# Optimization experiments

Measured on AMD Instinct MI355X. Metric: run time of the kernel, lower is better.

Reference implementation:

```python
import jax, jax.numpy as jnp
import numpy as np

D_MODEL = 1024
N_HEADS = 16
D_K = D_MODEL // N_HEADS
SCALE = float(np.sqrt(D_K))


def depthwise3(x, w, b):
    # x: [B, S, D]; w: [D, 3] (PyTorch Conv1d weight [D,1,3] squeezed); b: [D]
    # cross-correlation with kernel_size=3, padding=1, groups=D
    xp = jnp.pad(x, ((0, 0), (1, 1), (0, 0)))
    return xp[:, :-2] * w[:, 0] + xp[:, 1:-1] * w[:, 1] + xp[:, 2:] * w[:, 2] + b


def setup_inputs() -> dict:
    key = jax.random.key(0)
    ks = jax.random.split(key, 16)
    B, S, D = 2, 2048, D_MODEL
    s_lin = 1.0 / np.sqrt(D)
    s_dw = 1.0 / np.sqrt(3)
    inp = {
        "x": jax.random.normal(ks[0], (B, S, D), dtype=jnp.float32),
        "dwq_w": jax.random.uniform(ks[1], (D, 3), jnp.float32, -s_dw, s_dw),
        "dwq_b": jax.random.uniform(ks[2], (D,), jnp.float32, -s_dw, s_dw),
        "dwk_w": jax.random.uniform(ks[3], (D, 3), jnp.float32, -s_dw, s_dw),
        "dwk_b": jax.random.uniform(ks[4], (D,), jnp.float32, -s_dw, s_dw),
        "dwv_w": jax.random.uniform(ks[5], (D, 3), jnp.float32, -s_dw, s_dw),
        "dwv_b": jax.random.uniform(ks[6], (D,), jnp.float32, -s_dw, s_dw),
        "wq": jax.random.uniform(ks[7], (D, D), jnp.float32, -s_lin, s_lin),
        "bq": jax.random.uniform(ks[8], (D,), jnp.float32, -s_lin, s_lin),
        "wk": jax.random.uniform(ks[9], (D, D), jnp.float32, -s_lin, s_lin),
        "bk": jax.random.uniform(ks[10], (D,), jnp.float32, -s_lin, s_lin),
        "wv": jax.random.uniform(ks[11], (D, D), jnp.float32, -s_lin, s_lin),
        "bv": jax.random.uniform(ks[12], (D,), jnp.float32, -s_lin, s_lin),
        "wo": jax.random.uniform(ks[13], (D, D), jnp.float32, -s_lin, s_lin),
        "bo": jax.random.uniform(ks[14], (D,), jnp.float32, -s_lin, s_lin),
    }
    return inp


def reference(x, dwq_w, dwq_b, dwk_w, dwk_b, dwv_w, dwv_b,
              wq, bq, wk, bk, wv, bv, wo, bo):
    B, S, D = x.shape
    # depthwise conv (k=3, pad=1) then linear projection (PyTorch: y = x @ W^T + b)
    q = depthwise3(x, dwq_w, dwq_b) @ wq.T + bq
    k = depthwise3(x, dwk_w, dwk_b) @ wk.T + bk
    v = depthwise3(x, dwv_w, dwv_b) @ wv.T + bv
    # [B, H, S, d_k]
    q = q.reshape(B, S, N_HEADS, D_K).transpose(0, 2, 1, 3)
    k = k.reshape(B, S, N_HEADS, D_K).transpose(0, 2, 1, 3)
    v = v.reshape(B, S, N_HEADS, D_K).transpose(0, 2, 1, 3)
    scores = jnp.einsum("bhqd,bhkd->bhqk", q, k) / SCALE
    attn = jax.nn.softmax(scores, axis=-1)  # dropout=0 (eval)
    out = jnp.einsum("bhqk,bhkd->bhqd", attn, v)
    out = out.transpose(0, 2, 1, 3).reshape(B, S, D)
    return out @ wo.T + bo
```

## Files before the change

### kernel.cpp

```cpp
#include <hip/hip_runtime.h>

typedef __bf16 bf16x8 __attribute__((ext_vector_type(8)));
typedef float f32x4 __attribute__((ext_vector_type(4)));
typedef float f32x16 __attribute__((ext_vector_type(16)));
typedef unsigned short u16x8 __attribute__((ext_vector_type(8)));
typedef unsigned short u16x4 __attribute__((ext_vector_type(4)));
typedef unsigned int u32x2 __attribute__((ext_vector_type(2)));

__device__ __forceinline__ unsigned short f2bf(float f) {
  union { float f; unsigned int u; } v; v.f = f;
  unsigned int r = v.u + 0x7FFFu + ((v.u >> 16) & 1u);
  return (unsigned short)(r >> 16);
}

__device__ __forceinline__ void gload_lds16(const void* g, void* l) {
  __builtin_amdgcn_global_load_lds(
      (const __attribute__((address_space(1))) void*)g,
      (__attribute__((address_space(3))) void*)l, 16, 0, 0);
}

__global__ __launch_bounds__(256)
void prep_kernel(const float* __restrict__ x,
                 const float* __restrict__ wq3, const float* __restrict__ bq3,
                 const float* __restrict__ wk3, const float* __restrict__ bk3,
                 const float* __restrict__ wv3, const float* __restrict__ bv3,
                 unsigned short* __restrict__ cq, unsigned short* __restrict__ ck,
                 unsigned short* __restrict__ cv,
                 const float* __restrict__ wq, const float* __restrict__ wk,
                 const float* __restrict__ wv, const float* __restrict__ wo,
                 unsigned short* __restrict__ wqb, unsigned short* __restrict__ wkb,
                 unsigned short* __restrict__ wvb, unsigned short* __restrict__ wob)
{
  if (blockIdx.x >= 4096) {
    int bb = blockIdx.x - 4096;
    const float* src; unsigned short* dst;
    switch (bb >> 10) {
      case 0: src = wq; dst = wqb; break;
      case 1: src = wk; dst = wkb; break;
      case 2: src = wv; dst = wvb; break;
      default: src = wo; dst = wob; break;
    }
    int i = (bb & 1023) * 1024 + threadIdx.x * 4;
    f32x4 v = *(const f32x4*)(src + i);
    u16x4 o;
    #pragma unroll
    for (int j = 0; j < 4; j++) o[j] = f2bf(v[j]);
    *(u16x4*)(dst + i) = o;
    return;
  }
  int t = blockIdx.x;
  int s = t & 2047;
  int d0 = threadIdx.x * 4;
  int base = t * 1024 + d0;
  f32x4 xc = *(const f32x4*)(x + base);
  f32x4 xm = (s > 0)    ? *(const f32x4*)(x + base - 1024) : f32x4{0.f,0.f,0.f,0.f};
  f32x4 xp = (s < 2047) ? *(const f32x4*)(x + base + 1024) : f32x4{0.f,0.f,0.f,0.f};

  #pragma unroll
  for (int path = 0; path < 3; path++) {
    const float* wP = (path == 0) ? wq3 : ((path == 1) ? wk3 : wv3);
    const float* bP = (path == 0) ? bq3 : ((path == 1) ? bk3 : bv3);
    unsigned short* oP = (path == 0) ? cq : ((path == 1) ? ck : cv);
    f32x4 w0 = *(const f32x4*)(wP + d0*3);
    f32x4 w1 = *(const f32x4*)(wP + d0*3 + 4);
    f32x4 w2 = *(const f32x4*)(wP + d0*3 + 8);
    f32x4 b4 = *(const f32x4*)(bP + d0);
    u16x4 o;
    #pragma unroll
    for (int dd = 0; dd < 4; dd++) {
      float wa, wb, wc;
      int j0 = dd*3, j1 = dd*3+1, j2 = dd*3+2;
      wa = (j0 < 4) ? w0[j0] : ((j0 < 8) ? w1[j0-4] : w2[j0-8]);
      wb = (j1 < 4) ? w0[j1] : ((j1 < 8) ? w1[j1-4] : w2[j1-8]);
      wc = (j2 < 4) ? w0[j2] : ((j2 < 8) ? w1[j2-4] : w2[j2-8]);
      o[dd] = f2bf(xm[dd]*wa + xc[dd]*wb + xp[dd]*wc + b4[dd]);
    }
    *(u16x4*)(oP + base) = o;
  }
}

__global__ __launch_bounds__(256, 3)
void gemm_qkv_kernel(const unsigned short* __restrict__ cq, const unsigned short* __restrict__ ck,
                     const unsigned short* __restrict__ cv,
                     const unsigned short* __restrict__ wqb, const unsigned short* __restrict__ wkb,
                     const unsigned short* __restrict__ wvb,
                     const float* __restrict__ bq, const float* __restrict__ bk,
                     const float* __restrict__ bv,
                     unsigned short* __restrict__ qo, unsigned short* __restrict__ ko,
                     unsigned short* __restrict__ vtb)
{
  const int K = 1024;
  __shared__ alignas(16) unsigned short lA[3 * 4096];
  __shared__ alignas(16) unsigned short lB[3 * 4096];
  int z = blockIdx.z;
  const unsigned short* A = (z == 0) ? cq : ((z == 1) ? ck : cv);
  const unsigned short* W = (z == 0) ? wqb : ((z == 1) ? wkb : wvb);
  const float* bias       = (z == 0) ? bq : ((z == 1) ? bk : bv);
  float scale             = (z == 0) ? 0.125f * 1.4426950408889634f : 1.0f;

  int bm = blockIdx.y * 128, bn = blockIdx.x * 128;
  const int tid = threadIdx.x, lane = tid & 63, w = tid >> 6;
  const int lrow = lane & 15, lgrp = lane >> 4;
  const int wm = (w >> 1) * 64, wn = (w & 1) * 64;

  f32x4 acc[4][4];
  #pragma unroll
  for (int i = 0; i < 4; i++)
    #pragma unroll
    for (int j = 0; j < 4; j++) acc[i][j] = f32x4{0.f,0.f,0.f,0.f};

  auto STAGE = [&](int buf, int k0) {
    #pragma unroll
    for (int c = 0; c < 2; c++) {
      int slot_base = c * 256 + w * 64;
      int slot = slot_base + lane;
      int row = slot >> 2;
      int kc8 = ((slot & 3) ^ (row & 3)) << 3;
      gload_lds16(A + (size_t)(bm + row) * K + k0 + kc8, lA + buf * 4096 + slot_base * 8);
      gload_lds16(W + (size_t)(bn + row) * K + k0 + kc8, lB + buf * 4096 + slot_base * 8);
    }
  };

  STAGE(0, 0);
  STAGE(1, 32);
  int cur = 0, stg = 2;

  for (int t = 0; t < 32; t++) {
    if (t < 31) { asm volatile("s_waitcnt vmcnt(4)" ::: "memory"); }
    else        { asm volatile("s_waitcnt vmcnt(0)" ::: "memory"); }
    __builtin_amdgcn_s_barrier();
    __builtin_amdgcn_sched_barrier(0);
    if (t + 2 < 32) STAGE(stg, (t + 2) * 32);

    bf16x8 af[4], bfr[4];
    #pragma unroll
    for (int mt = 0; mt < 4; mt++) {
      int rr = wm + mt*16 + lrow;
      af[mt] = *(const bf16x8*)(lA + cur*4096 + (rr << 5) + ((lgrp ^ (rr & 3)) << 3));
    }
    #pragma unroll
    for (int nt = 0; nt < 4; nt++) {
      int rr = wn + nt*16 + lrow;
      bfr[nt] = *(const bf16x8*)(lB + cur*4096 + (rr << 5) + ((lgrp ^ (rr & 3)) << 3));
    }
    #pragma unroll
    for (int mt = 0; mt < 4; mt++)
      #pragma unroll
      for (int nt = 0; nt < 4; nt++)
        acc[mt][nt] = __builtin_amdgcn_mfma_f32_16x16x32_bf16(af[mt], bfr[nt], acc[mt][nt], 0, 0, 0);

    cur = (cur == 2) ? 0 : cur + 1;
    stg = (stg == 2) ? 0 : stg + 1;
  }

  if (z == 2) {
    #pragma unroll
    for (int mt = 0; mt < 4; mt++) {
      #pragma unroll
      for (int nt = 0; nt < 4; nt++) {
        int gn = bn + wn + nt*16 + lrow;
        float bb = bias[gn];
        int h = gn >> 6, dk = gn & 63;
        int gm0 = bm + wm + mt*16 + lgrp*4;
        int b = gm0 >> 11, s0 = gm0 & 2047;
        u16x4 pk;
        #pragma unroll
        for (int i = 0; i < 4; i++) pk[i] = f2bf(acc[mt][nt][i] + bb);
        unsigned short* dst = vtb +
            ((((size_t)(b*16 + h)) * 32 + (s0 >> 6)) * 64 + dk) * 64 + (s0 & 63);
        *(u16x4*)dst = pk;
      }
    }
  } else {
    unsigned short* O = (z == 0) ? qo : ko;
    #pragma unroll
    for (int mt = 0; mt < 4; mt++) {
      #pragma unroll
      for (int nt = 0; nt < 4; nt++) {
        int gn = bn + wn + nt*16 + lrow;
        float bb = bias[gn];
        int h = gn >> 6, dk = gn & 63;
        #pragma unroll
        for (int i = 0; i < 4; i++) {
          int gm = bm + wm + mt*16 + lgrp*4 + i;
          int b = gm >> 11, s = gm & 2047;
          float val = (acc[mt][nt][i] + bb) * scale;
          O[((size_t)(b*16 + h) * 2048 + s) * 64 + dk] = f2bf(val);
        }
      }
    }
  }
}

__global__ __launch_bounds__(256)
void gemm_out_kernel(const unsigned short* __restrict__ A, const unsigned short* __restrict__ W,
                     const float* __restrict__ bias, float* __restrict__ Out)
{
  const int K = 1024;
  __shared__ alignas(16) unsigned short lA[3 * 2048];
  __shared__ alignas(16) unsigned short lB[3 * 4096];
  int bm = blockIdx.y * 64, bn = blockIdx.x * 128;
  const int tid = threadIdx.x, lane = tid & 63, w = tid >> 6;
  const int lrow = lane & 15, lgrp = lane >> 4;
  const int wm = (w >> 1) * 32, wn = (w & 1) * 64;

  f32x4 acc[2][4];
  #pragma unroll
  for (int mt = 0; mt < 2; mt++)
    #pragma unroll
    for (int nt = 0; nt < 4; nt++) acc[mt][nt] = f32x4{0.f,0.f,0.f,0.f};

  auto STAGE = [&](int buf, int k0) {
    {
      int slot = tid;
      int row = slot >> 2;
      int kc8 = ((slot & 3) ^ (row & 3)) << 3;
      gload_lds16(A + (size_t)(bm + row) * K + k0 + kc8, lA + buf * 2048 + (w * 64) * 8);
    }
    #pragma unroll
    for (int c = 0; c < 2; c++) {
      int slot_base = c * 256 + w * 64;
      int slot = slot_base + lane;
      int row = slot >> 2;
      int kc8 = ((slot & 3) ^ (row & 3)) << 3;
      gload_lds16(W + (size_t)(bn + row) * K + k0 + kc8, lB + buf * 4096 + slot_base * 8);
    }
  };

  STAGE(0, 0);
  STAGE(1, 32);
  int cur = 0, stg = 2;

  for (int t = 0; t < 32; t++) {
    if (t < 31) { asm volatile("s_waitcnt vmcnt(3)" ::: "memory"); }
    else        { asm volatile("s_waitcnt vmcnt(0)" ::: "memory"); }
    __builtin_amdgcn_s_barrier();
    __builtin_amdgcn_sched_barrier(0);
    if (t + 2 < 32) STAGE(stg, (t + 2) * 32);

    bf16x8 af[2], bfr[4];
    #pragma unroll
    for (int mt = 0; mt < 2; mt++) {
      int rr = wm + mt*16 + lrow;
      af[mt] = *(const bf16x8*)(lA + cur*2048 + (rr << 5) + ((lgrp ^ (rr & 3)) << 3));
    }
    #pragma unroll
    for (int nt = 0; nt < 4; nt++) {
      int rr = wn + nt*16 + lrow;
      bfr[nt] = *(const bf16x8*)(lB + cur*4096 + (rr << 5) + ((lgrp ^ (rr & 3)) << 3));
    }
    #pragma unroll
    for (int mt = 0; mt < 2; mt++)
      #pragma unroll
      for (int nt = 0; nt < 4; nt++)
        acc[mt][nt] = __builtin_amdgcn_mfma_f32_16x16x32_bf16(af[mt], bfr[nt], acc[mt][nt], 0, 0, 0);

    cur = (cur == 2) ? 0 : cur + 1;
    stg = (stg == 2) ? 0 : stg + 1;
  }

  #pragma unroll
  for (int mt = 0; mt < 2; mt++) {
    #pragma unroll
    for (int nt = 0; nt < 4; nt++) {
      int gn = bn + wn + nt*16 + lrow;
      float bb = bias[gn];
      #pragma unroll
      for (int i = 0; i < 4; i++) {
        int gm = bm + wm + mt*16 + lgrp*4 + i;
        Out[(size_t)gm * 1024 + gn] = acc[mt][nt][i] + bb;
      }
    }
  }
}

__global__ __launch_bounds__(256, 2)
void attn_kernel(const unsigned short* __restrict__ Q, const unsigned short* __restrict__ K,
                 const unsigned short* __restrict__ Vtb, unsigned short* __restrict__ O)
{
  const int S = 2048, NT = 32;
  int n = blockIdx.x;
  int xcd = n & 7, r = n >> 3;
  int bh = (xcd << 2) | (r & 3);
  int qbase = (r >> 2) * 128;

  const int tid = threadIdx.x, lane = tid & 63, w = tid >> 6;
  const int lq = lane & 31;
  const int lh = lane >> 5;
  const unsigned short* Qh = Q   + (size_t)bh * S * 64;
  const unsigned short* Kh = K   + (size_t)bh * S * 64;
  const unsigned short* Vh = Vtb + (size_t)bh * 32 * 4096;

  __shared__ alignas(16) unsigned short Kb[3][4096];
  __shared__ alignas(16) unsigned short Vb[3][4096];

  bf16x8 qf[4];
  {
    const unsigned short* qp = Qh + (size_t)(qbase + w*32 + lq) * 64 + lh * 8;
    #pragma unroll
    for (int ks = 0; ks < 4; ks++)
      qf[ks] = *(const bf16x8*)(qp + ks * 16);
  }

  f32x16 oacc[2];
  #pragma unroll
  for (int i = 0; i < 16; i++) { oacc[0][i] = 0.f; oacc[1][i] = 0.f; }
  float lsum = 0.f;

  auto STAGE = [&](int buf, int gt) {
    const unsigned short* gK = Kh + (size_t)gt * 4096;
    const unsigned short* gV = Vh + (size_t)gt * 4096;
    #pragma unroll
    for (int c = 0; c < 2; c++) {
      int slot_base = c * 256 + w * 64;
      int slot = slot_base + lane;
      int row = slot >> 3;
      int srcoff = (row << 6) + (((slot & 7) ^ (row & 7)) << 3);
      gload_lds16(gK + srcoff, &Kb[buf][slot_base * 8]);
      gload_lds16(gV + srcoff, &Vb[buf][slot_base * 8]);
    }
  };

  STAGE(0, 0);
  STAGE(1, 1);
  int cur = 0, stg = 2;

  for (int t = 0; t < NT; t++) {
    if (t < NT - 1) { asm volatile("s_waitcnt vmcnt(4)" ::: "memory"); }
    else            { asm volatile("s_waitcnt vmcnt(0)" ::: "memory"); }
    __builtin_amdgcn_s_barrier();
    __builtin_amdgcn_sched_barrier(0);

    if (t + 2 < NT) STAGE(stg, t + 2);

    f32x16 sacc[2];
    #pragma unroll
    for (int i = 0; i < 16; i++) { sacc[0][i] = 0.f; sacc[1][i] = 0.f; }
    #pragma unroll
    for (int ks = 0; ks < 4; ks++) {
      #pragma unroll
      for (int kt = 0; kt < 2; kt++) {
        int row = kt*32 + lq;
        bf16x8 kf = *(const bf16x8*)(&Kb[cur][(row << 6) + ((((ks<<1)+lh) ^ (row & 7)) << 3)]);
        sacc[kt] = __builtin_amdgcn_mfma_f32_32x32x16_bf16(kf, qf[ks], sacc[kt], 0, 0, 0);
      }
    }

    bf16x8 pa[4];
    #pragma unroll
    for (int kp = 0; kp < 4; kp++) {
      const int sv = kp >> 1;
      const int rb = (kp & 1) * 8;
      float p[8];
      #pragma unroll
      for (int i = 0; i < 8; i++)
        p[i] = __builtin_amdgcn_exp2f(sacc[sv][rb + i]);
      lsum += ((p[0]+p[1]) + (p[2]+p[3])) + ((p[4]+p[5]) + (p[6]+p[7]));
      unsigned int X, Y, Z, W2;
      asm("v_cvt_pk_bf16_f32 %0, %1, %2" : "=v"(X)  : "v"(p[0]), "v"(p[1]));
      asm("v_cvt_pk_bf16_f32 %0, %1, %2" : "=v"(Y)  : "v"(p[2]), "v"(p[3]));
      asm("v_cvt_pk_bf16_f32 %0, %1, %2" : "=v"(Z)  : "v"(p[4]), "v"(p[5]));
      asm("v_cvt_pk_bf16_f32 %0, %1, %2" : "=v"(W2) : "v"(p[6]), "v"(p[7]));
      u32x2 rxz = __builtin_amdgcn_permlane32_swap(X, Z, false, false);
      u32x2 ryw = __builtin_amdgcn_permlane32_swap(Y, W2, false, false);
      union { unsigned int u[4]; bf16x8 v; } pk;
      pk.u[0] = rxz[0]; pk.u[1] = ryw[0]; pk.u[2] = rxz[1]; pk.u[3] = ryw[1];
      pa[kp] = pk.v;
    }

    __builtin_amdgcn_s_setprio(1);
    #pragma unroll
    for (int kp = 0; kp < 4; kp++) {
      #pragma unroll
      for (int dt = 0; dt < 2; dt++) {
        int row = dt*32 + lq;
        bf16x8 vf = *(const bf16x8*)(&Vb[cur][(row << 6) + ((((kp<<1)+lh) ^ (row & 7)) << 3)]);
        oacc[dt] = __builtin_amdgcn_mfma_f32_32x32x16_bf16(pa[kp], vf, oacc[dt], 0, 0, 0);
      }
    }
    __builtin_amdgcn_s_setprio(0);

    cur = (cur == 2) ? 0 : cur + 1;
    stg = (stg == 2) ? 0 : stg + 1;
  }

  float ltot = lsum + __shfl_xor(lsum, 32, 64);

  int b = bh >> 4, h = bh & 15;
  #pragma unroll
  for (int reg = 0; reg < 16; reg++) {
    int qrl = (reg & 3) + 8*(reg >> 2) + 4*lh;
    float lq_ = __shfl(ltot, qrl, 64);
    float rl = 1.0f / lq_;
    int qrow = qbase + w*32 + qrl;
    unsigned short* dst = O + ((size_t)(b*2048 + qrow)) * 1024 + h*64 + lq;
    dst[0]  = f2bf(oacc[0][reg] * rl);
    dst[32] = f2bf(oacc[1][reg] * rl);
  }
}

extern "C" void kernel_launch(void* const* d_in, const int* in_sizes, int n_in,
                              void* d_out, int out_size, void* d_ws, size_t ws_size,
                              hipStream_t stream)
{
  const float* x     = (const float*)d_in[0];
  const float* dwq_w = (const float*)d_in[1];
  const float* dwq_b = (const float*)d_in[2];
  const float* dwk_w = (const float*)d_in[3];
  const float* dwk_b = (const float*)d_in[4];
  const float* dwv_w = (const float*)d_in[5];
  const float* dwv_b = (const float*)d_in[6];
  const float* wq    = (const float*)d_in[7];
  const float* bq    = (const float*)d_in[8];
  const float* wk    = (const float*)d_in[9];
  const float* bk    = (const float*)d_in[10];
  const float* wv    = (const float*)d_in[11];
  const float* bv    = (const float*)d_in[12];
  const float* wo    = (const float*)d_in[13];
  const float* bo    = (const float*)d_in[14];
  float* out = (float*)d_out;

  char* ws = (char*)d_ws;
  const size_t MB = 1024 * 1024;
  unsigned short* cq  = (unsigned short*)(ws + 0);
  unsigned short* ck  = (unsigned short*)(ws + 8*MB);
  unsigned short* cv  = (unsigned short*)(ws + 16*MB);
  unsigned short* qd  = (unsigned short*)(ws + 24*MB);
  unsigned short* kd  = (unsigned short*)(ws + 32*MB);
  unsigned short* wqb = (unsigned short*)(ws + 48*MB);
  unsigned short* wkb = (unsigned short*)(ws + 50*MB);
  unsigned short* wvb = (unsigned short*)(ws + 52*MB);
  unsigned short* wob = (unsigned short*)(ws + 54*MB);
  unsigned short* attn_out = cq;
  unsigned short* vtb      = ck;

  prep_kernel<<<8192, 256, 0, stream>>>(x, dwq_w, dwq_b, dwk_w, dwk_b, dwv_w, dwv_b,
                                        cq, ck, cv, wq, wk, wv, wo, wqb, wkb, wvb, wob);
  gemm_qkv_kernel<<<dim3(8, 32, 3), 256, 0, stream>>>(cq, ck, cv, wqb, wkb, wvb, bq, bk, bv, qd, kd, vtb);
  attn_kernel<<<512, 256, 0, stream>>>(qd, kd, vtb, attn_out);
  gemm_out_kernel<<<dim3(8, 64), 256, 0, stream>>>(attn_out, wob, bo, out);
}
```

Before: 127.1 us.

## Software-pipeline QK of next tile with softmax/PV of current tile

Restructures the attention loop to compute the QK^T scores for tile t+1 before doing exp and PV for tile t, alternating two score register sets. LDS staging grows from 3 to 4 buffers and prefetches three tiles ahead. The goal is to overlap MFMA work with the exp/convert VALU work and hide load latency. In exchange it uses more LDS (64KB per block), which may reduce occupancy, and more registers for the second score accumulator.

New measurement: 127.4 us. Within noise of the previous version (+0.2%).

```diff
diff --git a/kernel.cpp b/kernel.cpp
--- a/kernel.cpp
+++ b/kernel.cpp
@@ -291,8 +291,8 @@
   const unsigned short* Kh = K   + (size_t)bh * S * 64;
   const unsigned short* Vh = Vtb + (size_t)bh * 32 * 4096;
 
-  __shared__ alignas(16) unsigned short Kb[3][4096];
-  __shared__ alignas(16) unsigned short Vb[3][4096];
+  __shared__ alignas(16) unsigned short Kb[4][4096];
+  __shared__ alignas(16) unsigned short Vb[4][4096];
 
   bf16x8 qf[4];
   {
@@ -321,31 +321,21 @@
     }
   };
 
-  STAGE(0, 0);
-  STAGE(1, 1);
-  int cur = 0, stg = 2;
-
-  for (int t = 0; t < NT; t++) {
-    if (t < NT - 1) { asm volatile("s_waitcnt vmcnt(4)" ::: "memory"); }
-    else            { asm volatile("s_waitcnt vmcnt(0)" ::: "memory"); }
-    __builtin_amdgcn_s_barrier();
-    __builtin_amdgcn_sched_barrier(0);
-
-    if (t + 2 < NT) STAGE(stg, t + 2);
-
-    f32x16 sacc[2];
-    #pragma unroll
-    for (int i = 0; i < 16; i++) { sacc[0][i] = 0.f; sacc[1][i] = 0.f; }
+  auto QK = [&](int kt1, f32x16 (&s)[2]) {
+    #pragma unroll
+    for (int i = 0; i < 16; i++) { s[0][i] = 0.f; s[1][i] = 0.f; }
     #pragma unroll
     for (int ks = 0; ks < 4; ks++) {
       #pragma unroll
       for (int kt = 0; kt < 2; kt++) {
         int row = kt*32 + lq;
-        bf16x8 kf = *(const bf16x8*)(&Kb[cur][(row << 6) + ((((ks<<1)+lh) ^ (row & 7)) << 3)]);
-        sacc[kt] = __builtin_amdgcn_mfma_f32_32x32x16_bf16(kf, qf[ks], sacc[kt], 0, 0, 0);
+        bf16x8 kf = *(const bf16x8*)(&Kb[kt1 & 3][(row << 6) + ((((ks<<1)+lh) ^ (row & 7)) << 3)]);
+        s[kt] = __builtin_amdgcn_mfma_f32_32x32x16_bf16(kf, qf[ks], s[kt], 0, 0, 0);
       }
     }
-
+  };
+
+  auto EXPPV = [&](int t, f32x16 (&s)[2]) {
     bf16x8 pa[4];
     #pragma unroll
     for (int kp = 0; kp < 4; kp++) {
@@ -354,7 +344,7 @@
       float p[8];
       #pragma unroll
       for (int i = 0; i < 8; i++)
-        p[i] = __builtin_amdgcn_exp2f(sacc[sv][rb + i]);
+        p[i] = __builtin_amdgcn_exp2f(s[sv][rb + i]);
       lsum += ((p[0]+p[1]) + (p[2]+p[3])) + ((p[4]+p[5]) + (p[6]+p[7]));
       unsigned int X, Y, Z, W2;
       asm("v_cvt_pk_bf16_f32 %0, %1, %2" : "=v"(X)  : "v"(p[0]), "v"(p[1]));
@@ -367,21 +357,45 @@
       pk.u[0] = rxz[0]; pk.u[1] = ryw[0]; pk.u[2] = rxz[1]; pk.u[3] = ryw[1];
       pa[kp] = pk.v;
     }
-
     __builtin_amdgcn_s_setprio(1);
     #pragma unroll
     for (int kp = 0; kp < 4; kp++) {
       #pragma unroll
       for (int dt = 0; dt < 2; dt++) {
         int row = dt*32 + lq;
-        bf16x8 vf = *(const bf16x8*)(&Vb[cur][(row << 6) + ((((kp<<1)+lh) ^ (row & 7)) << 3)]);
+        bf16x8 vf = *(const bf16x8*)(&Vb[t & 3][(row << 6) + ((((kp<<1)+lh) ^ (row & 7)) << 3)]);
         oacc[dt] = __builtin_amdgcn_mfma_f32_32x32x16_bf16(pa[kp], vf, oacc[dt], 0, 0, 0);
       }
     }
     __builtin_amdgcn_s_setprio(0);
-
-    cur = (cur == 2) ? 0 : cur + 1;
-    stg = (stg == 2) ? 0 : stg + 1;
+  };
+
+  STAGE(0, 0);
+  STAGE(1, 1);
+  STAGE(2, 2);
+  asm volatile("s_waitcnt vmcnt(8)" ::: "memory");
+  __builtin_amdgcn_s_barrier();
+  __builtin_amdgcn_sched_barrier(0);
+
+  f32x16 sA[2], sB[2];
+  QK(0, sA);
+
+  for (int t = 0; t < NT; t += 2) {
+    if (t < NT - 2) { asm volatile("s_waitcnt vmcnt(4)" ::: "memory"); }
+    else            { asm volatile("s_waitcnt vmcnt(0)" ::: "memory"); }
+    __builtin_amdgcn_s_barrier();
+    __builtin_amdgcn_sched_barrier(0);
+    if (t + 3 < NT) STAGE((t + 3) & 3, t + 3);
+    if (t + 1 < NT) QK(t + 1, sB);
+    EXPPV(t, sA);
+
+    if (t + 2 < NT - 1) { asm volatile("s_waitcnt vmcnt(4)" ::: "memory"); }
+    else                { asm volatile("s_waitcnt vmcnt(0)" ::: "memory"); }
+    __builtin_amdgcn_s_barrier();
+    __builtin_amdgcn_sched_barrier(0);
+    if (t + 4 < NT) STAGE((t + 4) & 3, t + 4);
+    if (t + 2 < NT) QK(t + 2, sA);
+    EXPPV(t + 1, sB);
   }
 
   float ltot = lsum + __shfl_xor(lsum, 32, 64);
```
